# Kernel tuning notes

Measured on AMD Instinct MI355X. Metric: run time of the kernel, lower is better.

The kernel has to match this reference:

```python
import jax, jax.numpy as jnp
import numpy as np

WS = (2, 7, 7)          # window shape (T, H, W)
NUM_HEADS = 4
DIM = 128
L_WINDOWS = 512         # windows per video sample (mask leading dim)


def _rel_pos_idx():
    # Static int index map [N, N] into the (2T-1)(2H-1)(2W-1)=507 bias table.
    t, h, w = WS
    coords = np.stack(np.meshgrid(np.arange(t), np.arange(h), np.arange(w), indexing='ij'))
    coords = coords.reshape(3, -1)                      # [3, N]
    rel = coords[:, :, None] - coords[:, None, :]       # [3, N, N]
    rel[0] += t - 1; rel[1] += h - 1; rel[2] += w - 1
    idx = rel[0] * (2 * h - 1) * (2 * w - 1) + rel[1] * (2 * w - 1) + rel[2]
    return jnp.asarray(idx, dtype=jnp.int32)            # [98, 98]

REL_IDX = _rel_pos_idx()


def setup_inputs() -> dict:
    key = jax.random.key(0)
    ks = jax.random.split(key, 6)
    B, N, C, H = 2048, 98, DIM, NUM_HEADS
    M = (2 * WS[0] - 1) * (2 * WS[1] - 1) * (2 * WS[2] - 1)  # 507
    return {
        'x': jax.random.normal(ks[0], (B, N, C), dtype=jnp.float32),
        'mask': jnp.zeros((L_WINDOWS, N, N), dtype=jnp.float32),
        'qkv_w': jax.random.normal(ks[1], (3 * C, C), dtype=jnp.float32) * 0.02,
        'qkv_b': jnp.zeros((3 * C,), dtype=jnp.float32),
        'rel_pos_embed': jax.random.normal(ks[2], (H, M), dtype=jnp.float32) * 0.02,
        'proj_w': jax.random.normal(ks[3], (C, C), dtype=jnp.float32) * 0.02,
        'proj_b': jnp.zeros((C,), dtype=jnp.float32),
    }


def reference(x, mask, qkv_w, qkv_b, rel_pos_embed, proj_w, proj_b):
    B, N, C = x.shape
    H = NUM_HEADS
    hd = C // H
    scale = hd ** -0.5

    qkv = x @ qkv_w.T + qkv_b                           # [B, N, 3C]
    qkv = qkv.reshape(B, N, 3, H, hd).transpose(2, 0, 3, 1, 4)  # [3, B, H, N, hd]
    q, k, v = qkv[0] * scale, qkv[1], qkv[2]

    attn = jnp.einsum('bhnd,bhmd->bhnm', q, k)          # [B, H, N, N]
    bias = rel_pos_embed[:, REL_IDX]                    # [H, N, N] gathered bias
    attn = attn + bias[None]

    L = mask.shape[0]
    attn = attn.reshape(B // L, L, H, N, N) + mask[None, :, None]
    attn = attn.reshape(B, H, N, N)

    attn = jax.nn.softmax(attn, axis=-1)
    out = jnp.einsum('bhnm,bhmd->bhnd', attn, v)        # [B, H, N, hd]
    out = out.transpose(0, 2, 1, 3).reshape(B, N, C)
    return out @ proj_w.T + proj_b
```

## Files before the change

kernel.cpp:

```cpp
#include <hip/hip_runtime.h>

typedef __attribute__((ext_vector_type(8))) _Float16 half8;
typedef __attribute__((ext_vector_type(16))) float f32x16;

#define TOK 98
#define QSCALE 0.17677669529663687f

#define XL   0
#define XSTR 132
#define VT   0
#define VSTR 132
#define QS   4224
#define KS   8144
#define PS   4224
#define PSTR 120
#define LDSH 15984

__device__ inline half8 cvt8(float4 a, float4 b) {
    half8 r;
    r[0] = (_Float16)a.x; r[1] = (_Float16)a.y; r[2] = (_Float16)a.z; r[3] = (_Float16)a.w;
    r[4] = (_Float16)b.x; r[5] = (_Float16)b.y; r[6] = (_Float16)b.z; r[7] = (_Float16)b.w;
    return r;
}

__global__ void prep_w(const float* __restrict__ qkv_w,
                       const float* __restrict__ proj_w,
                       _Float16* __restrict__ w16)
{
    int i = blockIdx.x * 256 + threadIdx.x;
    if (i < 49152) {
        int e = i & 7, lane = (i >> 3) & 63, kt = (i >> 9) & 7;
        int g = i >> 12;
        int h = g / 3, nt = g - 3 * h;
        int t32 = lane & 31, hf = lane >> 5;
        w16[i] = (_Float16)qkv_w[(nt * 128 + h * 32 + t32) * 128 + kt * 16 + hf * 8 + e];
    } else {
        int j = i - 49152;
        int e = j & 7, lane = (j >> 3) & 63, kt = (j >> 9) & 7, nt = j >> 12;
        int t32 = lane & 31, hf = lane >> 5;
        w16[i] = (_Float16)proj_w[(nt * 32 + t32) * 128 + kt * 16 + hf * 8 + e];
    }
}

__global__ __launch_bounds__(256, 4) void attn_mfma(
    const float* __restrict__ x,
    const float* __restrict__ mask,
    const float* __restrict__ qkv_b,
    const float* __restrict__ rel,
    const _Float16* __restrict__ qkv16,
    float* __restrict__ out,
    _Float16* __restrict__ o16,
    int Lmask, int useO16)
{
    __shared__ __align__(16) _Float16 lh[LDSH];
    __shared__ float rel_lds[507];

    const int tid  = threadIdx.x;

    int wg = (int)blockIdx.x;
    int work;
    if ((gridDim.x & 7) == 0) {
        int cpx = gridDim.x >> 3;
        work = (wg & 7) * cpx + (wg >> 3);
    } else {
        work = wg;
    }
    const int b    = work >> 2;
    const int h    = work & 3;

    const int wv   = tid >> 6;
    const int lane = tid & 63;
    const int t32  = lane & 31;
    const int half = lane >> 5;

    for (int i = tid; i < 507; i += 256) rel_lds[i] = rel[h * 507 + i];
    for (int j = tid; j < TOK * 16; j += 256) {
        int row = j >> 4, c8 = (j & 15) << 3;
        const float* src = x + ((long)b * TOK + row) * 128 + c8;
        float4 a0 = *(const float4*)src;
        float4 a1 = *(const float4*)(src + 4);
        *(half8*)&lh[XL + row * XSTR + c8] = cvt8(a0, a1);
    }
    __syncthreads();

    int tok = 32 * wv + t32; if (tok > 97) tok = 97;

    half8 af[8];
#pragma unroll
    for (int kt = 0; kt < 8; ++kt)
        af[kt] = *(const half8*)&lh[XL + tok * XSTR + kt * 16 + half * 8];

    __syncthreads();

    const _Float16* wbase = qkv16 + (long)h * 3 * 4096 + lane * 8;

    f32x16 acc[3];
#pragma unroll
    for (int nt = 0; nt < 3; nt++)
#pragma unroll
        for (int i = 0; i < 16; i++) acc[nt][i] = 0.f;

#pragma unroll
    for (int kt = 0; kt < 8; ++kt) {
#pragma unroll
        for (int nt = 0; nt < 3; nt++) {
            half8 bf = *(const half8*)(wbase + (nt * 8 + kt) * 512);
            acc[nt] = __builtin_amdgcn_mfma_f32_32x32x16_f16(af[kt], bf, acc[nt], 0, 0, 0);
        }
    }

    {
        const float qb = qkv_b[h * 32 + t32];
        const float kb = qkv_b[128 + h * 32 + t32];
        const float vb = qkv_b[256 + h * 32 + t32];
#pragma unroll
        for (int reg = 0; reg < 16; ++reg) {
            int m = 32 * wv + (reg & 3) + 8 * (reg >> 2) + 4 * half;
            if (m < TOK) {
                lh[QS + m * 40 + t32]   = (_Float16)((acc[0][reg] + qb) * QSCALE);
                lh[KS + m * 40 + t32]   = (_Float16)(acc[1][reg] + kb);
                lh[VT + t32 * VSTR + m] = (_Float16)(acc[2][reg] + vb);
            }
        }
    }
    for (int i = tid; i < 32 * 14; i += 256) {
        int d = i / 14, m = i - 14 * d;
        lh[VT + d * VSTR + 98 + m] = (_Float16)0.f;
    }

    const long mbase = (long)(b % Lmask) * (TOK * TOK);
    const int mrow0 = 32 * wv + 4 * half;

    int jterm[4]; bool jvld[4];
    float mv[4][16];
#pragma unroll
    for (int nt = 0; nt < 4; ++nt) {
        int j = nt * 32 + t32;
        jvld[nt] = (j < TOK);
        int jc = jvld[nt] ? j : 97;
        int tj = jc / 49; int rj = jc - 49 * tj; int hj = rj / 7; int wj = rj - 7 * hj;
        jterm[nt] = tj * 169 + hj * 13 + wj;
        const float* mc = mask + mbase + jc;
#pragma unroll
        for (int reg = 0; reg < 16; ++reg) {
            int m = mrow0 + (reg & 3) + 8 * (reg >> 2);
            int mm = m > 97 ? 97 : m;
            mv[nt][reg] = mc[(long)mm * TOK];
        }
    }

    __syncthreads();

    f32x16 sacc[4];
#pragma unroll
    for (int reg = 0; reg < 16; ++reg) {
        int m = mrow0 + (reg & 3) + 8 * (reg >> 2);
        bool mok = (m < TOK);
        int mm = mok ? m : 97;
        int ti = mm / 49; int r2 = mm - 49 * ti; int hi = r2 / 7; int wi = r2 - 7 * hi;
        int mterm = ti * 169 + hi * 13 + wi + 253;
#pragma unroll
        for (int nt = 0; nt < 4; ++nt) {
            float s = -1e30f;
            if (mok && jvld[nt]) s = rel_lds[mterm - jterm[nt]] + mv[nt][reg];
            sacc[nt][reg] = s;
        }
    }

#pragma unroll
    for (int kk = 0; kk < 2; ++kk) {
        half8 qa = *(const half8*)&lh[QS + tok * 40 + kk * 16 + half * 8];
#pragma unroll
        for (int nt = 0; nt < 4; ++nt) {
            int kr = nt * 32 + t32; if (kr > 97) kr = 97;
            half8 kf = *(const half8*)&lh[KS + kr * 40 + kk * 16 + half * 8];
            sacc[nt] = __builtin_amdgcn_mfma_f32_32x32x16_f16(qa, kf, sacc[nt], 0, 0, 0);
        }
    }

    __syncthreads();

    float wm = -1e30f;
#pragma unroll
    for (int nt = 0; nt < 4; ++nt)
#pragma unroll
        for (int reg = 0; reg < 16; ++reg) wm = fmaxf(wm, sacc[nt][reg]);
    wm = fmaxf(wm, __shfl_xor(wm, 1));
    wm = fmaxf(wm, __shfl_xor(wm, 2));
    wm = fmaxf(wm, __shfl_xor(wm, 4));
    wm = fmaxf(wm, __shfl_xor(wm, 8));
    wm = fmaxf(wm, __shfl_xor(wm, 16));
    wm = fmaxf(wm, __shfl_xor(wm, 32));

#pragma unroll
    for (int nt = 0; nt < 4; ++nt) {
        int j = nt * 32 + t32;
#pragma unroll
        for (int reg = 0; reg < 16; ++reg) {
            int m = mrow0 + (reg & 3) + 8 * (reg >> 2);
            float p = __expf(sacc[nt][reg] - wm);
            if (m < TOK && j < 112) lh[PS + m * PSTR + j] = (_Float16)p;
        }
    }

    f32x16 oacc, osum;
#pragma unroll
    for (int i = 0; i < 16; i++) { oacc[i] = 0.f; osum[i] = 0.f; }

    half8 vones;
#pragma unroll
    for (int i = 0; i < 8; ++i) vones[i] = (_Float16)1.0f;

#pragma unroll
    for (int kk = 0; kk < 7; ++kk) {
        half8 pa = *(const half8*)&lh[PS + tok * PSTR + kk * 16 + half * 8];
        half8 vf = *(const half8*)&lh[VT + t32 * VSTR + kk * 16 + half * 8];
        oacc = __builtin_amdgcn_mfma_f32_32x32x16_f16(pa, vf, oacc, 0, 0, 0);
        osum = __builtin_amdgcn_mfma_f32_32x32x16_f16(pa, vones, osum, 0, 0, 0);
    }

    if (useO16) {
        _Float16* ob = o16 + ((long)b * TOK) * 128 + h * 32 + t32;
#pragma unroll
        for (int reg = 0; reg < 16; ++reg) {
            int m = mrow0 + (reg & 3) + 8 * (reg >> 2);
            float inv = __builtin_amdgcn_rcpf(osum[reg]);
            if (m < TOK) ob[(long)m * 128] = (_Float16)(oacc[reg] * inv);
        }
    } else {
        float* ob = out + ((long)b * TOK) * 128 + h * 32 + t32;
#pragma unroll
        for (int reg = 0; reg < 16; ++reg) {
            int m = mrow0 + (reg & 3) + 8 * (reg >> 2);
            float inv = __builtin_amdgcn_rcpf(osum[reg]);
            if (m < TOK) ob[(long)m * 128] = oacc[reg] * inv;
        }
    }
}

template <bool A16>
__global__ __launch_bounds__(256, 4) void proj_mfma(
    const void* __restrict__ Ain,
    const _Float16* __restrict__ w16,
    const float* __restrict__ proj_b,
    float* __restrict__ out,
    int totalRows)
{
    __shared__ __align__(16) _Float16 al[128 * 132];

    const int tid  = threadIdx.x;
    const int wv   = tid >> 6;
    const int lane = tid & 63;
    const int t32  = lane & 31;
    const int half = lane >> 5;

#pragma unroll
    for (int it = 0; it < 8; ++it) {
        int j = it * 256 + tid;
        int row = j >> 4, c8 = (j & 15) << 3;
        long gr = (long)blockIdx.x * 128 + row;
        if (gr >= totalRows) gr = totalRows - 1;
        if (A16) {
            *(half8*)&al[row * 132 + c8] =
                *(const half8*)((const _Float16*)Ain + gr * 128 + c8);
        } else {
            const float* src = (const float*)Ain + gr * 128 + c8;
            float4 a0 = *(const float4*)src;
            float4 a1 = *(const float4*)(src + 4);
            *(half8*)&al[row * 132 + c8] = cvt8(a0, a1);
        }
    }
    __syncthreads();

    half8 af[8];
#pragma unroll
    for (int kt = 0; kt < 8; ++kt)
        af[kt] = *(const half8*)&al[(32 * wv + t32) * 132 + kt * 16 + half * 8];

    const _Float16* wb = w16 + lane * 8;

    f32x16 acc[4];
#pragma unroll
    for (int nt = 0; nt < 4; nt++)
#pragma unroll
        for (int i = 0; i < 16; i++) acc[nt][i] = 0.f;

#pragma unroll
    for (int kt = 0; kt < 8; ++kt) {
#pragma unroll
        for (int nt = 0; nt < 4; ++nt) {
            half8 bf = *(const half8*)(wb + (nt * 8 + kt) * 512);
            acc[nt] = __builtin_amdgcn_mfma_f32_32x32x16_f16(af[kt], bf, acc[nt], 0, 0, 0);
        }
    }

    const long rowb = (long)blockIdx.x * 128 + 32 * wv;
#pragma unroll
    for (int nt = 0; nt < 4; ++nt) {
        int co = nt * 32 + t32;
        float pb = proj_b[co];
#pragma unroll
        for (int reg = 0; reg < 16; ++reg) {
            long m = rowb + (reg & 3) + 8 * (reg >> 2) + 4 * half;
            if (m < totalRows) out[m * 128 + co] = acc[nt][reg] + pb;
        }
    }
}

extern "C" void kernel_launch(void* const* d_in, const int* in_sizes, int n_in,
                              void* d_out, int out_size, void* d_ws, size_t ws_size,
                              hipStream_t stream) {
    const float* x      = (const float*)d_in[0];
    const float* mask   = (const float*)d_in[1];
    const float* qkv_w  = (const float*)d_in[2];
    const float* qkv_b  = (const float*)d_in[3];
    const float* rel    = (const float*)d_in[4];
    const float* proj_w = (const float*)d_in[5];
    const float* proj_b = (const float*)d_in[6];
    float* out = (float*)d_out;

    const int B     = in_sizes[0] / (TOK * 128);
    const int Lmask = in_sizes[1] / (TOK * TOK);
    const int totalRows = B * TOK;

    _Float16* w16  = (_Float16*)d_ws;
    _Float16* o16  = w16 + 65536;
    const size_t needO = 131072 + (size_t)totalRows * 128 * 2;
    const int useO16 = (ws_size >= needO) ? 1 : 0;

    prep_w<<<256, 256, 0, stream>>>(qkv_w, proj_w, w16);

    attn_mfma<<<B * 4, 256, 0, stream>>>(x, mask, qkv_b, rel, w16, out, o16,
                                         Lmask, useO16);

    const int grid = (totalRows + 127) / 128;
    if (useO16)
        proj_mfma<true><<<grid, 256, 0, stream>>>((const void*)o16, w16 + 49152,
                                                  proj_b, out, totalRows);
    else
        proj_mfma<false><<<grid, 256, 0, stream>>>((const void*)out, w16 + 49152,
                                                   proj_b, out, totalRows);
}
```

Before: 356.5 us.

## Precompute gathered relative-position bias table in prep kernel and prefetch earlier

The prep kernel now expands the relative-position bias into a dense per-head [98 x 112] float table in workspace. The attention kernel reads bias values straight from global memory alongside the mask, instead of staging the 507-entry table in LDS and computing gather indices per element. Those mask and bias loads are moved before the QKV MFMA loop so their latency can overlap the matmul. Launch bounds rise to 5 waves per SIMD, and stores skip bounds checks for fully valid waves. The cost is 64 extra live registers for the bias values, which may pressure the new occupancy target, plus extra global traffic for the bias table.

```diff
diff --git a/kernel.cpp b/kernel.cpp
--- a/kernel.cpp
+++ b/kernel.cpp
@@ -16,6 +16,8 @@
 #define PSTR 120
 #define LDSH 15984
 
+#define BIAS_STR 112
+
 __device__ inline half8 cvt8(float4 a, float4 b) {
     half8 r;
     r[0] = (_Float16)a.x; r[1] = (_Float16)a.y; r[2] = (_Float16)a.z; r[3] = (_Float16)a.w;
@@ -25,7 +27,9 @@
 
 __global__ void prep_w(const float* __restrict__ qkv_w,
                        const float* __restrict__ proj_w,
-                       _Float16* __restrict__ w16)
+                       const float* __restrict__ rel,
+                       _Float16* __restrict__ w16,
+                       float* __restrict__ bias32)
 {
     int i = blockIdx.x * 256 + threadIdx.x;
     if (i < 49152) {
@@ -34,26 +38,38 @@
         int h = g / 3, nt = g - 3 * h;
         int t32 = lane & 31, hf = lane >> 5;
         w16[i] = (_Float16)qkv_w[(nt * 128 + h * 32 + t32) * 128 + kt * 16 + hf * 8 + e];
-    } else {
+    } else if (i < 65536) {
         int j = i - 49152;
         int e = j & 7, lane = (j >> 3) & 63, kt = (j >> 9) & 7, nt = j >> 12;
         int t32 = lane & 31, hf = lane >> 5;
         w16[i] = (_Float16)proj_w[(nt * 32 + t32) * 128 + kt * 16 + hf * 8 + e];
-    }
-}
-
-__global__ __launch_bounds__(256, 4) void attn_mfma(
+    } else if (i < 65536 + 4 * 98 * BIAS_STR) {
+        int j0 = i - 65536;
+        int jj = j0 % BIAS_STR;
+        int t  = j0 / BIAS_STR;
+        int m  = t % 98, h = t / 98;
+        float v = 0.f;
+        if (jj < 98) {
+            int ti = m / 49,  r2 = m - 49 * ti,  hi = r2 / 7,  wi = r2 - 7 * hi;
+            int tj = jj / 49, rj = jj - 49 * tj, hj = rj / 7, wj = rj - 7 * hj;
+            int idx = (ti - tj + 1) * 169 + (hi - hj + 6) * 13 + (wi - wj + 6);
+            v = rel[h * 507 + idx];
+        }
+        bias32[j0] = v;
+    }
+}
+
+__global__ __launch_bounds__(256, 5) void attn_mfma(
     const float* __restrict__ x,
     const float* __restrict__ mask,
     const float* __restrict__ qkv_b,
-    const float* __restrict__ rel,
     const _Float16* __restrict__ qkv16,
+    const float* __restrict__ bias32,
     float* __restrict__ out,
     _Float16* __restrict__ o16,
     int Lmask, int useO16)
 {
     __shared__ __align__(16) _Float16 lh[LDSH];
-    __shared__ float rel_lds[507];
 
     const int tid  = threadIdx.x;
 
@@ -73,7 +89,6 @@
     const int t32  = lane & 31;
     const int half = lane >> 5;
 
-    for (int i = tid; i < 507; i += 256) rel_lds[i] = rel[h * 507 + i];
     for (int j = tid; j < TOK * 16; j += 256) {
         int row = j >> 4, c8 = (j & 15) << 3;
         const float* src = x + ((long)b * TOK + row) * 128 + c8;
@@ -90,6 +105,27 @@
     for (int kt = 0; kt < 8; ++kt)
         af[kt] = *(const half8*)&lh[XL + tok * XSTR + kt * 16 + half * 8];
 
+    const long mbase = (long)(b % Lmask) * (TOK * TOK);
+    const int mrow0 = 32 * wv + 4 * half;
+
+    bool jvld[4];
+    float mv[4][16], bv[4][16];
+#pragma unroll
+    for (int nt = 0; nt < 4; ++nt) {
+        int j = nt * 32 + t32;
+        jvld[nt] = (j < TOK);
+        int jc = jvld[nt] ? j : 97;
+        const float* mc = mask + mbase + jc;
+        const float* bc = bias32 + (h * 98) * BIAS_STR + jc;
+#pragma unroll
+        for (int reg = 0; reg < 16; ++reg) {
+            int m = mrow0 + (reg & 3) + 8 * (reg >> 2);
+            int mm = m > 97 ? 97 : m;
+            mv[nt][reg] = mc[(long)mm * TOK];
+            bv[nt][reg] = bc[mm * BIAS_STR];
+        }
+    }
+
     __syncthreads();
 
     const _Float16* wbase = qkv16 + (long)h * 3 * 4096 + lane * 8;
@@ -113,14 +149,25 @@
         const float qb = qkv_b[h * 32 + t32];
         const float kb = qkv_b[128 + h * 32 + t32];
         const float vb = qkv_b[256 + h * 32 + t32];
-#pragma unroll
-        for (int reg = 0; reg < 16; ++reg) {
-            int m = 32 * wv + (reg & 3) + 8 * (reg >> 2) + 4 * half;
-            if (m < TOK) {
+        const bool allv = (32 * wv + 31) < TOK;
+        if (allv) {
+#pragma unroll
+            for (int reg = 0; reg < 16; ++reg) {
+                int m = 32 * wv + (reg & 3) + 8 * (reg >> 2) + 4 * half;
                 lh[QS + m * 40 + t32]   = (_Float16)((acc[0][reg] + qb) * QSCALE);
                 lh[KS + m * 40 + t32]   = (_Float16)(acc[1][reg] + kb);
                 lh[VT + t32 * VSTR + m] = (_Float16)(acc[2][reg] + vb);
             }
+        } else {
+#pragma unroll
+            for (int reg = 0; reg < 16; ++reg) {
+                int m = 32 * wv + (reg & 3) + 8 * (reg >> 2) + 4 * half;
+                if (m < TOK) {
+                    lh[QS + m * 40 + t32]   = (_Float16)((acc[0][reg] + qb) * QSCALE);
+                    lh[KS + m * 40 + t32]   = (_Float16)(acc[1][reg] + kb);
+                    lh[VT + t32 * VSTR + m] = (_Float16)(acc[2][reg] + vb);
+                }
+            }
         }
     }
     for (int i = tid; i < 32 * 14; i += 256) {
@@ -128,27 +175,6 @@
         lh[VT + d * VSTR + 98 + m] = (_Float16)0.f;
     }
 
-    const long mbase = (long)(b % Lmask) * (TOK * TOK);
-    const int mrow0 = 32 * wv + 4 * half;
-
-    int jterm[4]; bool jvld[4];
-    float mv[4][16];
-#pragma unroll
-    for (int nt = 0; nt < 4; ++nt) {
-        int j = nt * 32 + t32;
-        jvld[nt] = (j < TOK);
-        int jc = jvld[nt] ? j : 97;
-        int tj = jc / 49; int rj = jc - 49 * tj; int hj = rj / 7; int wj = rj - 7 * hj;
-        jterm[nt] = tj * 169 + hj * 13 + wj;
-        const float* mc = mask + mbase + jc;
-#pragma unroll
-        for (int reg = 0; reg < 16; ++reg) {
-            int m = mrow0 + (reg & 3) + 8 * (reg >> 2);
-            int mm = m > 97 ? 97 : m;
-            mv[nt][reg] = mc[(long)mm * TOK];
-        }
-    }
-
     __syncthreads();
 
     f32x16 sacc[4];
@@ -156,15 +182,9 @@
     for (int reg = 0; reg < 16; ++reg) {
         int m = mrow0 + (reg & 3) + 8 * (reg >> 2);
         bool mok = (m < TOK);
-        int mm = mok ? m : 97;
-        int ti = mm / 49; int r2 = mm - 49 * ti; int hi = r2 / 7; int wi = r2 - 7 * hi;
-        int mterm = ti * 169 + hi * 13 + wi + 253;
-#pragma unroll
-        for (int nt = 0; nt < 4; ++nt) {
-            float s = -1e30f;
-            if (mok && jvld[nt]) s = rel_lds[mterm - jterm[nt]] + mv[nt][reg];
-            sacc[nt][reg] = s;
-        }
+#pragma unroll
+        for (int nt = 0; nt < 4; ++nt)
+            sacc[nt][reg] = (mok && jvld[nt]) ? bv[nt][reg] + mv[nt][reg] : -1e30f;
     }
 
 #pragma unroll
@@ -219,13 +239,14 @@
         osum = __builtin_amdgcn_mfma_f32_32x32x16_f16(pa, vones, osum, 0, 0, 0);
     }
 
+    const bool allv = (32 * wv + 31) < TOK;
     if (useO16) {
         _Float16* ob = o16 + ((long)b * TOK) * 128 + h * 32 + t32;
 #pragma unroll
         for (int reg = 0; reg < 16; ++reg) {
             int m = mrow0 + (reg & 3) + 8 * (reg >> 2);
             float inv = __builtin_amdgcn_rcpf(osum[reg]);
-            if (m < TOK) ob[(long)m * 128] = (_Float16)(oacc[reg] * inv);
+            if (allv || m < TOK) ob[(long)m * 128] = (_Float16)(oacc[reg] * inv);
         }
     } else {
         float* ob = out + ((long)b * TOK) * 128 + h * 32 + t32;
@@ -233,7 +254,7 @@
         for (int reg = 0; reg < 16; ++reg) {
             int m = mrow0 + (reg & 3) + 8 * (reg >> 2);
             float inv = __builtin_amdgcn_rcpf(osum[reg]);
-            if (m < TOK) ob[(long)m * 128] = oacc[reg] * inv;
+            if (allv || m < TOK) ob[(long)m * 128] = oacc[reg] * inv;
         }
     }
 }
@@ -323,14 +344,16 @@
     const int Lmask = in_sizes[1] / (TOK * TOK);
     const int totalRows = B * TOK;
 
-    _Float16* w16  = (_Float16*)d_ws;
-    _Float16* o16  = w16 + 65536;
-    const size_t needO = 131072 + (size_t)totalRows * 128 * 2;
+    _Float16* w16    = (_Float16*)d_ws;
+    float*    bias32 = (float*)((char*)d_ws + 131072);
+    _Float16* o16    = (_Float16*)((char*)d_ws + 131072 + 175616);
+    const size_t needO = 131072 + 175616 + (size_t)totalRows * 256;
     const int useO16 = (ws_size >= needO) ? 1 : 0;
 
-    prep_w<<<256, 256, 0, stream>>>(qkv_w, proj_w, w16);
-
-    attn_mfma<<<B * 4, 256, 0, stream>>>(x, mask, qkv_b, rel, w16, out, o16,
+    const int prepN = 65536 + 4 * 98 * BIAS_STR;
+    prep_w<<<(prepN + 255) / 256, 256, 0, stream>>>(qkv_w, proj_w, rel, w16, bias32);
+
+    attn_mfma<<<B * 4, 256, 0, stream>>>(x, mask, qkv_b, w16, bias32, out, o16,
                                          Lmask, useO16);
 
     const int grid = (totalRows + 127) / 128;
```

Result: slower. 1.423 ms (+299.1%).
